# Optimization experiments

Hardware: AMD Instinct MI355X
Metric: run time of the kernel (lower is better)

The kernel has to match this reference:

```python
import jax, jax.numpy as jnp
import numpy as np

FLOAT_EPS = float(np.finfo(np.float32).eps)  # matches torch.finfo(torch.float32).eps


def setup_inputs() -> dict:
    key = jax.random.key(0)
    k0, k1, k2, k3, k4 = jax.random.split(key, 5)
    B, P, I, O, L = 16, 8192, 256, 128, 256  # batch, points, in_shapes, out_shapes, RNN_LATENT_SIZE
    x = jax.random.uniform(k0, (B, P, I), dtype=jnp.float32)
    latent_vector = jax.random.normal(k1, (B, L), dtype=jnp.float32)
    comp1 = 0.1 * jax.random.normal(k2, (L, I, O), dtype=jnp.float32)  # nn.init.normal_(std=0.1)
    comp2 = 0.1 * jax.random.normal(k3, (L, I, O), dtype=jnp.float32)
    temperature = jnp.full((1,), 2.0, dtype=jnp.float32)  # init.constant_(2)
    u = jax.random.uniform(k4, (B, 2, 1, I, O), dtype=jnp.float32)  # gumbel base noise (rand_like)
    return {"x": x, "latent_vector": latent_vector, "comp1": comp1,
            "comp2": comp2, "temperature": temperature, "u": u}


def reference(x, latent_vector, comp1, comp2, temperature, u):
    # mask_l/r: [B, I, O], softmax over the in-shapes axis (dim=-2)
    mask_l = jax.nn.softmax(jnp.einsum('bl,lio->bio', latent_vector, comp1), axis=-2)
    mask_r = jax.nn.softmax(jnp.einsum('bl,lio->bio', latent_vector, comp2), axis=-2)
    mask = jnp.stack([mask_l, mask_r], axis=1)[:, :, None]  # [B, 2, 1, I, O]

    # gumbel-softmax sampling: temperature clamp(eps, 2) then clamp_min(0.001)
    temp = jnp.maximum(jnp.clip(temperature, FLOAT_EPS, 2.0), 0.001)  # shape (1,)
    g = -jnp.log(-jnp.log(jnp.maximum(u, FLOAT_EPS)))
    mask_s = jax.nn.softmax((jnp.log(mask + FLOAT_EPS) + g) / temp, axis=-2)  # [B,2,1,I,O]

    # select: per-head broadcast-multiply-reduce == batched GEMM [B,P,I] x [B,2,I,O]
    sel = jnp.einsum('bpi,bkio->bpko', x, mask_s[:, :, 0])  # [B, P, 2, O]
    a, b = sel[:, :, 0], sel[:, :, 1]

    # arithmetic combine (union, intersection-ish, diffs) + clamp
    out = jnp.concatenate([a + b, a + b - 1.0, a - b, b - a], axis=-1)  # [B, P, 4*O]
    return jnp.clip(out, 0.0, 1.0)
```

## Files before the change

kernel.cpp:

```cpp
#include <hip/hip_runtime.h>
#include <hip/hip_bf16.h>

#define FLOAT_EPS 1.1920928955078125e-07f

typedef float f32x4 __attribute__((ext_vector_type(4)));
typedef short s16x8 __attribute__((ext_vector_type(8)));

#define B_ 16
#define P_ 8192
#define I_ 256
#define O_ 128
#define L_ 256
#define IO_ (I_*O_)

__device__ __forceinline__ float clip01(float v) {
    return fminf(fmaxf(v, 0.0f), 1.0f);
}
__device__ __forceinline__ f32x4 clip01v(f32x4 v) {
    f32x4 r;
    r[0] = clip01(v[0]); r[1] = clip01(v[1]);
    r[2] = clip01(v[2]); r[3] = clip01(v[3]);
    return r;
}

__global__ __launch_bounds__(256) void rl_k1_logits(
        const float* __restrict__ lat,
        const float* __restrict__ c1, const float* __restrict__ c2,
        float* __restrict__ lgP) {
    const int n  = blockIdx.x * 256 + threadIdx.x;
    const int ks = blockIdx.y;
    const int lh = blockIdx.z;
    const float* __restrict__ C  = (ks ? c2 : c1) + (size_t)lh * 128 * IO_;
    const int lbase = lh * 128;

    float acc[16];
#pragma unroll
    for (int b = 0; b < 16; ++b) acc[b] = 0.0f;

#pragma unroll 4
    for (int l = 0; l < 128; ++l) {
        float cv = C[(size_t)l * IO_ + n];
#pragma unroll
        for (int b = 0; b < 16; ++b)
            acc[b] += lat[b * L_ + lbase + l] * cv;
    }
    float* o = lgP + ((size_t)(lh * 32 + ks * 16)) * IO_ + n;
#pragma unroll
    for (int b = 0; b < 16; ++b) o[(size_t)b * IO_] = acc[b];
}

__global__ __launch_bounds__(256) void rl_k2_mask(
        const float* __restrict__ lgP, const float* __restrict__ u,
        const float* __restrict__ temp_p, __hip_bfloat16* __restrict__ MT) {
    const int oo = threadIdx.x & 15;
    const int g  = threadIdx.x >> 4;
    const int o0 = blockIdx.x * 16;
    const int ks = blockIdx.y;
    const int b  = blockIdx.z;

    __shared__ float slab[I_][16];
    __shared__ float red[16][16];

    const float* __restrict__ z0 = lgP + (size_t)(ks * 16 + b) * IO_ + o0 + oo;
    const float* __restrict__ z1 = z0 + (size_t)32 * IO_;
    const float* __restrict__ up = u + ((size_t)b * 2 + ks) * IO_ + o0 + oo;

    float T = temp_p[0];
    T = fminf(fmaxf(T, FLOAT_EPS), 2.0f);
    T = fmaxf(T, 0.001f);
    const float rT = 1.0f / T;

    const int i0 = g * 16, i1 = i0 + 16;

    for (int i = i0; i < i1; ++i)
        slab[i][oo] = z0[(size_t)i * O_] + z1[(size_t)i * O_];
    __syncthreads();

    float m = -INFINITY;
    for (int i = i0; i < i1; ++i) m = fmaxf(m, slab[i][oo]);
    red[g][oo] = m; __syncthreads();
    m = -INFINITY;
#pragma unroll
    for (int j = 0; j < 16; ++j) m = fmaxf(m, red[j][oo]);
    __syncthreads();

    float S = 0.0f;
    for (int i = i0; i < i1; ++i) S += expf(slab[i][oo] - m);
    red[g][oo] = S; __syncthreads();
    S = 0.0f;
#pragma unroll
    for (int j = 0; j < 16; ++j) S += red[j][oo];
    __syncthreads();
    const float invS = 1.0f / S;

    float m2 = -INFINITY;
    for (int i = i0; i < i1; ++i) {
        float p  = expf(slab[i][oo] - m) * invS;
        float uu = fmaxf(up[(size_t)i * O_], FLOAT_EPS);
        float gg = -logf(-logf(uu));
        float s  = (logf(p + FLOAT_EPS) + gg) * rT;
        slab[i][oo] = s;
        m2 = fmaxf(m2, s);
    }
    red[g][oo] = m2; __syncthreads();
    m2 = -INFINITY;
#pragma unroll
    for (int j = 0; j < 16; ++j) m2 = fmaxf(m2, red[j][oo]);
    __syncthreads();

    float S2 = 0.0f;
    for (int i = i0; i < i1; ++i) S2 += expf(slab[i][oo] - m2);
    red[g][oo] = S2; __syncthreads();
    S2 = 0.0f;
#pragma unroll
    for (int j = 0; j < 16; ++j) S2 += red[j][oo];
    const float invS2 = 1.0f / S2;

    __hip_bfloat16* __restrict__ row = MT + ((size_t)(b * 256 + ks * 128 + o0 + oo)) * I_;
    for (int i = i0; i < i1; i += 2) {
        float v0 = expf(slab[i][oo]     - m2) * invS2;
        float v1 = expf(slab[i + 1][oo] - m2) * invS2;
        __hip_bfloat162 pk = __float22bfloat162_rn(make_float2(v0, v1));
        *(__hip_bfloat162*)(row + i) = pk;
    }
}

__global__ __launch_bounds__(512, 2) void rl_k3_gemm(
        const float* __restrict__ X, const __hip_bfloat16* __restrict__ MT,
        float* __restrict__ OUT) {
    const int tid  = threadIdx.x;
    const int lane = tid & 63, wid = tid >> 6;
    const int b    = blockIdx.y;

    __shared__ short Blds[256 * 256];

    const float* __restrict__ Xb           = X   + (size_t)b * P_ * I_;
    const __hip_bfloat16* __restrict__ MTb = MT  + (size_t)b * 65536;
    float* __restrict__ Ob                 = OUT + (size_t)b * P_ * 512;

    const int l15 = lane & 15, lhi = lane >> 4;
    const int rowbase = blockIdx.x * 512 + wid * 64 + l15;

#pragma unroll
    for (int it = 0; it < 16; ++it) {
        int idx = it * 512 + tid;
        int n = idx >> 5, c = idx & 31;
        s16x8 v = *(const s16x8*)(MTb + n * 256 + c * 8);
        *(s16x8*)((char*)Blds + n * 512 + ((c * 16) ^ ((n & 7) << 4))) = v;
    }

    float4 raw[16];
    {
        const float* s0 = Xb + (size_t)rowbase * I_ + lhi * 8;
#pragma unroll
        for (int kk = 0; kk < 8; ++kk) {
            raw[2 * kk]     = *(const float4*)(s0 + kk * 32);
            raw[2 * kk + 1] = *(const float4*)(s0 + kk * 32 + 4);
        }
    }
    __syncthreads();

    for (int c = 0; c < 4; ++c) {
        s16x8 af[8];
#pragma unroll
        for (int kk = 0; kk < 8; ++kk) {
            float4 f0 = raw[2 * kk], f1 = raw[2 * kk + 1];
            union { s16x8 v; __hip_bfloat162 h[4]; } cv;
            cv.h[0] = __float22bfloat162_rn(make_float2(f0.x, f0.y));
            cv.h[1] = __float22bfloat162_rn(make_float2(f0.z, f0.w));
            cv.h[2] = __float22bfloat162_rn(make_float2(f1.x, f1.y));
            cv.h[3] = __float22bfloat162_rn(make_float2(f1.z, f1.w));
            af[kk] = cv.v;
        }
        if (c < 3) {
            const float* s1 = Xb + (size_t)(rowbase + (c + 1) * 16) * I_ + lhi * 8;
#pragma unroll
            for (int kk = 0; kk < 8; ++kk) {
                raw[2 * kk]     = *(const float4*)(s1 + kk * 32);
                raw[2 * kk + 1] = *(const float4*)(s1 + kk * 32 + 4);
            }
        }
        __builtin_amdgcn_sched_barrier(0);

        const int prow = blockIdx.x * 512 + wid * 64 + c * 16 + l15;
        float* __restrict__ oprow = Ob + (size_t)prow * 512 + lhi * 4;

#pragma unroll
        for (int fn = 0; fn < 8; ++fn) {
            f32x4 acc_a = (f32x4){0.f, 0.f, 0.f, 0.f};
            f32x4 acc_b = (f32x4){0.f, 0.f, 0.f, 0.f};
            const int na = fn * 16 + l15;
            const int nb = na + 128;
            const char* rowA = (const char*)Blds + na * 512;
            const char* rowB = (const char*)Blds + nb * 512;
            const int swz = (na & 7) << 4;
#pragma unroll
            for (int kk = 0; kk < 8; ++kk) {
                const int kb = (kk * 64 + lhi * 16) ^ swz;
                s16x8 bfa = *(const s16x8*)(rowA + kb);
                s16x8 bfb = *(const s16x8*)(rowB + kb);
                acc_a = __builtin_amdgcn_mfma_f32_16x16x32_bf16(bfa, af[kk], acc_a, 0, 0, 0);
                acc_b = __builtin_amdgcn_mfma_f32_16x16x32_bf16(bfb, af[kk], acc_b, 0, 0, 0);
            }
            f32x4 s = acc_a + acc_b;
            float* op = oprow + fn * 16;
            __builtin_nontemporal_store(clip01v(s),             (f32x4*)(op));
            __builtin_nontemporal_store(clip01v(s - 1.0f),      (f32x4*)(op + 128));
            __builtin_nontemporal_store(clip01v(acc_a - acc_b), (f32x4*)(op + 256));
            __builtin_nontemporal_store(clip01v(acc_b - acc_a), (f32x4*)(op + 384));
        }
    }
}

extern "C" void kernel_launch(void* const* d_in, const int* in_sizes, int n_in,
                              void* d_out, int out_size, void* d_ws, size_t ws_size,
                              hipStream_t stream) {
    const float* x    = (const float*)d_in[0];
    const float* lat  = (const float*)d_in[1];
    const float* c1   = (const float*)d_in[2];
    const float* c2   = (const float*)d_in[3];
    const float* temp = (const float*)d_in[4];
    const float* u    = (const float*)d_in[5];
    float* out = (float*)d_out;

    char* ws = (char*)d_ws;
    float*          lgP = (float*)ws;
    __hip_bfloat16* MT  = (__hip_bfloat16*)(ws + (8 << 20));

    rl_k1_logits<<<dim3(128, 2, 2), 256, 0, stream>>>(lat, c1, c2, lgP);
    rl_k2_mask  <<<dim3(8, 2, 16), 256, 0, stream>>>(lgP, u, temp, MT);
    rl_k3_gemm  <<<dim3(16, 16), 512, 0, stream>>>(x, MT, out);
}
```

Baseline: 138.2 us.

## Pre-swizzle mask into MFMA fragment order to simplify LDS reads

The mask kernel now writes the bf16 mask directly in the per-lane MFMA B-fragment order: 16-byte vectors grouped by 16-column tile, k-chunk and lane. The GEMM kernel copies that buffer linearly into LDS and reads each fragment as pA[kk*64] with no XOR swizzle arithmetic, so consecutive lanes hit consecutive 16-byte words. This removes per-read address computation and relies on the linear layout being free of LDS bank conflicts. The cost is that the producer and consumer kernels are now tightly coupled through this layout.

```diff
diff --git a/kernel.cpp b/kernel.cpp
--- a/kernel.cpp
+++ b/kernel.cpp
@@ -51,7 +51,7 @@
 
 __global__ __launch_bounds__(256) void rl_k2_mask(
         const float* __restrict__ lgP, const float* __restrict__ u,
-        const float* __restrict__ temp_p, __hip_bfloat16* __restrict__ MT) {
+        const float* __restrict__ temp_p, __hip_bfloat16* __restrict__ MTF) {
     const int oo = threadIdx.x & 15;
     const int g  = threadIdx.x >> 4;
     const int o0 = blockIdx.x * 16;
@@ -116,37 +116,45 @@
     for (int j = 0; j < 16; ++j) S2 += red[j][oo];
     const float invS2 = 1.0f / S2;
 
-    __hip_bfloat16* __restrict__ row = MT + ((size_t)(b * 256 + ks * 128 + o0 + oo)) * I_;
-    for (int i = i0; i < i1; i += 2) {
-        float v0 = expf(slab[i][oo]     - m2) * invS2;
-        float v1 = expf(slab[i + 1][oo] - m2) * invS2;
-        __hip_bfloat162 pk = __float22bfloat162_rn(make_float2(v0, v1));
-        *(__hip_bfloat162*)(row + i) = pk;
-    }
+    const int n  = ks * 128 + o0 + oo;
+    const int f  = n >> 4;
+    const int j0 = (f * 8 + (g >> 1)) * 64 + (g & 1) * 32 + oo;
+    s16x8* __restrict__ MTFb = (s16x8*)MTF + (size_t)b * 8192;
+
+    union { s16x8 v; __hip_bfloat162 h[4]; } c0, c1;
+#pragma unroll
+    for (int e = 0; e < 8; e += 2) {
+        float v0 = expf(slab[i0 + e][oo]     - m2) * invS2;
+        float v1 = expf(slab[i0 + e + 1][oo] - m2) * invS2;
+        c0.h[e >> 1] = __float22bfloat162_rn(make_float2(v0, v1));
+        float w0 = expf(slab[i0 + 8 + e][oo]     - m2) * invS2;
+        float w1 = expf(slab[i0 + 8 + e + 1][oo] - m2) * invS2;
+        c1.h[e >> 1] = __float22bfloat162_rn(make_float2(w0, w1));
+    }
+    MTFb[j0]      = c0.v;
+    MTFb[j0 + 16] = c1.v;
 }
 
 __global__ __launch_bounds__(512, 2) void rl_k3_gemm(
-        const float* __restrict__ X, const __hip_bfloat16* __restrict__ MT,
+        const float* __restrict__ X, const __hip_bfloat16* __restrict__ MTF,
         float* __restrict__ OUT) {
     const int tid  = threadIdx.x;
     const int lane = tid & 63, wid = tid >> 6;
     const int b    = blockIdx.y;
 
-    __shared__ short Blds[256 * 256];
-
-    const float* __restrict__ Xb           = X   + (size_t)b * P_ * I_;
-    const __hip_bfloat16* __restrict__ MTb = MT  + (size_t)b * 65536;
-    float* __restrict__ Ob                 = OUT + (size_t)b * P_ * 512;
+    __shared__ s16x8 BF[8192];
+
+    const float* __restrict__ Xb    = X + (size_t)b * P_ * I_;
+    const s16x8* __restrict__ MTFb  = (const s16x8*)MTF + (size_t)b * 8192;
+    float* __restrict__ Ob          = OUT + (size_t)b * P_ * 512;
 
     const int l15 = lane & 15, lhi = lane >> 4;
     const int rowbase = blockIdx.x * 512 + wid * 64 + l15;
 
 #pragma unroll
     for (int it = 0; it < 16; ++it) {
-        int idx = it * 512 + tid;
-        int n = idx >> 5, c = idx & 31;
-        s16x8 v = *(const s16x8*)(MTb + n * 256 + c * 8);
-        *(s16x8*)((char*)Blds + n * 512 + ((c * 16) ^ ((n & 7) << 4))) = v;
+        int j = it * 512 + tid;
+        BF[j] = MTFb[j];
     }
 
     float4 raw[16];
@@ -189,16 +197,12 @@
         for (int fn = 0; fn < 8; ++fn) {
             f32x4 acc_a = (f32x4){0.f, 0.f, 0.f, 0.f};
             f32x4 acc_b = (f32x4){0.f, 0.f, 0.f, 0.f};
-            const int na = fn * 16 + l15;
-            const int nb = na + 128;
-            const char* rowA = (const char*)Blds + na * 512;
-            const char* rowB = (const char*)Blds + nb * 512;
-            const int swz = (na & 7) << 4;
+            const s16x8* pA = BF + (fn * 8) * 64 + lane;
+            const s16x8* pB = BF + ((fn + 8) * 8) * 64 + lane;
 #pragma unroll
             for (int kk = 0; kk < 8; ++kk) {
-                const int kb = (kk * 64 + lhi * 16) ^ swz;
-                s16x8 bfa = *(const s16x8*)(rowA + kb);
-                s16x8 bfb = *(const s16x8*)(rowB + kb);
+                s16x8 bfa = pA[kk * 64];
+                s16x8 bfb = pB[kk * 64];
                 acc_a = __builtin_amdgcn_mfma_f32_16x16x32_bf16(bfa, af[kk], acc_a, 0, 0, 0);
                 acc_b = __builtin_amdgcn_mfma_f32_16x16x32_bf16(bfb, af[kk], acc_b, 0, 0, 0);
             }
@@ -225,9 +229,9 @@
 
     char* ws = (char*)d_ws;
     float*          lgP = (float*)ws;
-    __hip_bfloat16* MT  = (__hip_bfloat16*)(ws + (8 << 20));
+    __hip_bfloat16* MTF = (__hip_bfloat16*)(ws + (8 << 20));
 
     rl_k1_logits<<<dim3(128, 2, 2), 256, 0, stream>>>(lat, c1, c2, lgP);
-    rl_k2_mask  <<<dim3(8, 2, 16), 256, 0, stream>>>(lgP, u, temp, MT);
-    rl_k3_gemm  <<<dim3(16, 16), 512, 0, stream>>>(x, MT, out);
-}
+    rl_k2_mask  <<<dim3(8, 2, 16), 256, 0, stream>>>(lgP, u, temp, MTF);
+    rl_k3_gemm  <<<dim3(16, 16), 512, 0, stream>>>(x, MTF, out);
+}
```

Result: no change. 138.5 us (+0.2%).
